# Performance work log

Measured on AMD Instinct MI355X. Metric: run time of the kernel, lower is better.

The kernel has to match this reference:

```python
import jax, jax.numpy as jnp
import numpy as np

N = 1024      # hidden_nodes (number of columns)
W = 128       # column_width
D = 1024      # input_dimension
F = W * N + N # per-column i-layer input size
SPARSITY = W / (W * (N - 1) + N) * 1.0  # modified_sparsity with total_neigbours=1


def setup_inputs() -> dict:
    key = jax.random.key(0)
    ks = jax.random.split(key, 10)
    s = lambda fan_in: 1.0 / np.sqrt(fan_in)
    x = jax.random.normal(ks[0], (D,), jnp.float32)
    hidden_state = jax.random.normal(ks[1], (N,), jnp.float32)
    W1 = jax.random.uniform(ks[2], (N, W, D), jnp.float32, -s(D), s(D))
    b1 = jax.random.uniform(ks[3], (N, W), jnp.float32, -s(D), s(D))
    W2 = jax.random.uniform(ks[4], (N, W, W), jnp.float32, -s(W), s(W))
    b2 = jax.random.uniform(ks[5], (N, W), jnp.float32, -s(W), s(W))
    Wi = jax.random.uniform(ks[6], (N, F), jnp.float32, -s(F), s(F))
    bi = jax.random.uniform(ks[7], (N,), jnp.float32, -s(F), s(F))
    # bernoulli mask, then force each column's own width-block to 1
    mask = (jax.random.uniform(ks[8], (N, F), jnp.float32) < SPARSITY).astype(jnp.float32)
    cols = jnp.arange(F)
    owner = jnp.where(cols < N * W, cols // W, -1)          # which column owns each feature slot
    block = (owner[None, :] == jnp.arange(N)[:, None]).astype(jnp.float32)
    mask = jnp.maximum(mask, block)
    pred = 0.1 * jax.random.normal(ks[9], (N,), jnp.float32)  # prediction_parameters ~ N(0, 0.1)
    return {"x": x, "hidden_state": hidden_state, "W1": W1, "b1": b1,
            "W2": W2, "b2": b2, "Wi": Wi, "bi": bi, "mask": mask, "pred": pred}


def reference(x, hidden_state, W1, b1, W2, b2, Wi, bi, mask, pred):
    # phase 1: per-column feature extractor (fc1 -> relu -> fc2 -> relu), batched over columns
    f1 = jax.nn.relu(jnp.einsum('nwd,d->nw', W1, x) + b1)        # [N, W]
    f2 = jax.nn.relu(jnp.einsum('nvw,nw->nv', W2, f1) + b2)      # [N, W]
    # phase 2: every column sees concat(all features, all hidden states)
    feat = jnp.concatenate([f2.reshape(-1), hidden_state])       # [F] = [N*W + N]
    i = jnp.tanh(jnp.einsum('nf,f->n', Wi * mask, feat) + bi)    # [N]
    h = hidden_state + i                                         # [N]
    y = jnp.sum(pred * h)                                        # scalar prediction
    return y, h
```

## Files before the change

kernel.cpp:

```cpp
#include <hip/hip_runtime.h>
#include <math.h>

#define NN 1024
#define WW 128
#define DD 1024
#define FF (NN * WW + NN)
#define NCHUNK 516
#define NWORD (NCHUNK * 4)

#define WS_BM_OFF  528384
#define WS_NEEDED  (WS_BM_OFF + (size_t)NN * NWORD * 8)

typedef float f32x4 __attribute__((ext_vector_type(4)));
typedef float f32x2 __attribute__((ext_vector_type(2)));

__device__ __forceinline__ f32x4 nt4(const float* p) {
    return __builtin_nontemporal_load(reinterpret_cast<const f32x4*>(p));
}
__device__ __forceinline__ f32x2 nt2(const float* p) {
    return __builtin_nontemporal_load(reinterpret_cast<const f32x2*>(p));
}
__device__ __forceinline__ float wred(float s) {
    #pragma unroll
    for (int m = 32; m > 0; m >>= 1) s += __shfl_xor(s, m, 64);
    return s;
}

__global__ __launch_bounds__(256) void colmlp(
    const float* __restrict__ x, const float* __restrict__ hidden,
    const float* __restrict__ W1, const float* __restrict__ b1,
    const float* __restrict__ W2, const float* __restrict__ b2,
    float* __restrict__ feat)
{
    __shared__ float f1_s[WW];
    const int n = blockIdx.x, tid = threadIdx.x, lane = tid & 63, w = tid >> 6;

    f32x4 xv0 = *reinterpret_cast<const f32x4*>(x +   0 + lane * 4);
    f32x4 xv1 = *reinterpret_cast<const f32x4*>(x + 256 + lane * 4);
    f32x4 xv2 = *reinterpret_cast<const f32x4*>(x + 512 + lane * 4);
    f32x4 xv3 = *reinterpret_cast<const f32x4*>(x + 768 + lane * 4);

    const float* W1n = W1 + (size_t)n * WW * DD;
    for (int g = 0; g < 4; ++g) {
        const float* rp = W1n + (size_t)(w * 32 + g * 8) * DD + lane * 4;
        float p[8];
        #pragma unroll
        for (int i = 0; i < 8; ++i) {
            const float* r = rp + (size_t)i * DD;
            f32x4 a = nt4(r) * xv0;
            a += nt4(r + 256) * xv1;
            a += nt4(r + 512) * xv2;
            a += nt4(r + 768) * xv3;
            p[i] = (a[0] + a[1]) + (a[2] + a[3]);
        }
        #pragma unroll
        for (int i = 0; i < 8; ++i) {
            const float s = wred(p[i]);
            if (lane == 0) {
                const int rr = w * 32 + g * 8 + i;
                const float v = s + b1[n * WW + rr];
                f1_s[rr] = v > 0.f ? v : 0.f;
            }
        }
    }
    __syncthreads();

    const float* W2n = W2 + (size_t)n * WW * WW;
    const f32x2 f1v = *reinterpret_cast<const f32x2*>(&f1_s[lane * 2]);
    for (int g = 0; g < 4; ++g) {
        float p[8];
        #pragma unroll
        for (int i = 0; i < 8; ++i) {
            const int rr = w * 32 + g * 8 + i;
            const f32x2 a = nt2(W2n + (size_t)rr * WW + lane * 2);
            p[i] = a[0] * f1v[0] + a[1] * f1v[1];
        }
        #pragma unroll
        for (int i = 0; i < 8; ++i) {
            const float s = wred(p[i]);
            if (lane == 0) {
                const int rr = w * 32 + g * 8 + i;
                const float v = s + b2[n * WW + rr];
                feat[n * WW + rr] = v > 0.f ? v : 0.f;
            }
        }
    }
    if (tid == 0) feat[NN * WW + n] = hidden[n];
}

__global__ __launch_bounds__(256) void maskscan(
    const float* __restrict__ mask, unsigned long long* __restrict__ bm)
{
    const int tid = threadIdx.x, lane = tid & 63, w = tid >> 6;
    const int wave_id = blockIdx.x * 4 + w;
    const int nwaves  = gridDim.x * 4;
    const int total   = NN * NCHUNK;
    #pragma unroll 2
    for (int c = wave_id; c < total; c += nwaves) {
        const f32x4 m = nt4(mask + (size_t)c * 256 + lane * 4);
        const unsigned long long b0 = __ballot(m[0] != 0.f);
        const unsigned long long b1 = __ballot(m[1] != 0.f);
        const unsigned long long b2 = __ballot(m[2] != 0.f);
        const unsigned long long b3 = __ballot(m[3] != 0.f);
        if (lane < 4) {
            const unsigned long long v = lane == 0 ? b0 : lane == 1 ? b1 : lane == 2 ? b2 : b3;
            bm[(size_t)c * 4 + lane] = v;
        }
    }
}

__global__ __launch_bounds__(256) void dotk(
    const unsigned long long* __restrict__ bm, const float* __restrict__ Wi,
    const float* __restrict__ feat, const float* __restrict__ bi,
    const float* __restrict__ hidden, float* __restrict__ out)
{
    const int n = blockIdx.x, tid = threadIdx.x;
    const unsigned long long* brow = bm + (size_t)n * NWORD;
    const float* wrow = Wi + (size_t)n * FF;
    float acc = 0.f;
    for (int wd = tid; wd < NWORD; wd += 256) {
        unsigned long long b = brow[wd];
        const int basef = (wd >> 2) * 256 + (wd & 3);
        while (b) {
            const int l = __builtin_ctzll(b);
            const int f = basef + l * 4;
            acc += wrow[f] * feat[f];
            b &= b - 1;
        }
    }
    acc = wred(acc);
    __shared__ float partial[4];
    if ((tid & 63) == 0) partial[tid >> 6] = acc;
    __syncthreads();
    if (tid == 0) {
        const float s = (partial[0] + partial[1]) + (partial[2] + partial[3]);
        out[1 + n] = hidden[n] + tanhf(s + bi[n]);
    }
}

__global__ __launch_bounds__(256) void predk(
    const float* __restrict__ pred, const float* __restrict__ h,
    float* __restrict__ out)
{
    const int tid = threadIdx.x;
    float acc = 0.f;
    for (int i = tid; i < NN; i += 256) acc += pred[i] * h[i];
    acc = wred(acc);
    __shared__ float partial[4];
    if ((tid & 63) == 0) partial[tid >> 6] = acc;
    __syncthreads();
    if (tid == 0) out[0] = (partial[0] + partial[1]) + (partial[2] + partial[3]);
}

__global__ __launch_bounds__(256) void feat_kernel(
    const float* __restrict__ x, const float* __restrict__ hidden,
    const float* __restrict__ W1, const float* __restrict__ b1,
    const float* __restrict__ W2, const float* __restrict__ b2,
    float* __restrict__ feat)
{
    const int n = blockIdx.x, tid = threadIdx.x, lane = tid & 63, wave = tid >> 6;
    __shared__ float x_s[DD];
    __shared__ float f1_s[WW];
    *reinterpret_cast<float4*>(x_s + tid * 4) = *reinterpret_cast<const float4*>(x + tid * 4);
    if (tid == 0) feat[NN * WW + n] = hidden[n];
    __syncthreads();
    const float* W1n = W1 + (size_t)n * WW * DD;
    for (int r = wave * 32; r < wave * 32 + 32; ++r) {
        const float* row = W1n + (size_t)r * DD;
        float4 acc = {0.f, 0.f, 0.f, 0.f};
        #pragma unroll
        for (int it = 0; it < 4; ++it) {
            const float4 a  = *reinterpret_cast<const float4*>(row + it * 256 + lane * 4);
            const float4 xv = *reinterpret_cast<const float4*>(x_s + it * 256 + lane * 4);
            acc.x += a.x * xv.x; acc.y += a.y * xv.y;
            acc.z += a.z * xv.z; acc.w += a.w * xv.w;
        }
        float s = wred((acc.x + acc.y) + (acc.z + acc.w));
        if (lane == 0) {
            float v = s + b1[n * WW + r];
            f1_s[r] = v > 0.f ? v : 0.f;
        }
    }
    __syncthreads();
    const float* W2n = W2 + (size_t)n * WW * WW;
    for (int r = wave * 32; r < wave * 32 + 32; ++r) {
        const float2 a = *reinterpret_cast<const float2*>(W2n + (size_t)r * WW + lane * 2);
        const float2 f = *reinterpret_cast<const float2*>(f1_s + lane * 2);
        float s = wred(a.x * f.x + a.y * f.y);
        if (lane == 0) {
            float v = s + b2[n * WW + r];
            feat[n * WW + r] = v > 0.f ? v : 0.f;
        }
    }
}

__global__ __launch_bounds__(256) void sparse_kernel(
    const float* __restrict__ Wi, const float* __restrict__ mask,
    const float* __restrict__ bi, const float* __restrict__ hidden,
    const float* __restrict__ feat, float* __restrict__ out)
{
    const int n = blockIdx.x, tid = threadIdx.x;
    const float* mrow = mask + (size_t)n * FF;
    const float* wrow = Wi   + (size_t)n * FF;
    float acc = 0.f;
    for (int it = 0; it < FF / 1024; ++it) {
        const int f = it * 1024 + tid * 4;
        const float4 m = *reinterpret_cast<const float4*>(mrow + f);
        if (m.x != 0.f) acc += wrow[f + 0] * m.x * feat[f + 0];
        if (m.y != 0.f) acc += wrow[f + 1] * m.y * feat[f + 1];
        if (m.z != 0.f) acc += wrow[f + 2] * m.z * feat[f + 2];
        if (m.w != 0.f) acc += wrow[f + 3] * m.w * feat[f + 3];
    }
    acc = wred(acc);
    __shared__ float partial[4];
    if ((tid & 63) == 0) partial[tid >> 6] = acc;
    __syncthreads();
    if (tid == 0) {
        const float s = (partial[0] + partial[1]) + (partial[2] + partial[3]);
        out[1 + n] = hidden[n] + tanhf(s + bi[n]);
    }
}

extern "C" void kernel_launch(void* const* d_in, const int* in_sizes, int n_in,
                              void* d_out, int out_size, void* d_ws, size_t ws_size,
                              hipStream_t stream) {
    const float* x      = (const float*)d_in[0];
    const float* hidden = (const float*)d_in[1];
    const float* W1     = (const float*)d_in[2];
    const float* b1     = (const float*)d_in[3];
    const float* W2     = (const float*)d_in[4];
    const float* b2     = (const float*)d_in[5];
    const float* Wi     = (const float*)d_in[6];
    const float* bi     = (const float*)d_in[7];
    const float* mask   = (const float*)d_in[8];
    const float* pred   = (const float*)d_in[9];

    float* out  = (float*)d_out;
    float* feat = (float*)d_ws;
    unsigned long long* bm = (unsigned long long*)((char*)d_ws + WS_BM_OFF);

    if (ws_size >= WS_NEEDED) {
        colmlp<<<NN, 256, 0, stream>>>(x, hidden, W1, b1, W2, b2, feat);
        maskscan<<<2048, 256, 0, stream>>>(mask, bm);
        dotk<<<NN, 256, 0, stream>>>(bm, Wi, feat, bi, hidden, out);
    } else {
        feat_kernel<<<NN, 256, 0, stream>>>(x, hidden, W1, b1, W2, b2, feat);
        sparse_kernel<<<NN, 256, 0, stream>>>(Wi, mask, bi, hidden, feat, out);
    }
    predk<<<1, 256, 0, stream>>>(pred, out + 1, out);
}
```

Before: 238.6 us.

## Fuse column MLP and mask bitmap scan into one interleaved launch

Merges the column-MLP kernel and the mask-to-bitmap scan kernel into a single 3072-block launch. Every third block computes one column's features, and the other two blocks per group each scan a contiguous range of mask chunks. The intent is to remove one kernel launch and its boundary and to let the compute-heavy W1 streaming overlap with the bandwidth-heavy mask scan. In exchange, each scanning wave now walks a fixed contiguous range with no loop unrolling, which replaces the earlier grid-stride pattern.

```diff
diff --git a/kernel.cpp b/kernel.cpp
--- a/kernel.cpp
+++ b/kernel.cpp
@@ -6,7 +6,9 @@
 #define DD 1024
 #define FF (NN * WW + NN)
 #define NCHUNK 516
+#define TOTCHUNK (NN * NCHUNK)
 #define NWORD (NCHUNK * 4)
+#define SCANWAVES 8192
 
 #define WS_BM_OFF  528384
 #define WS_NEEDED  (WS_BM_OFF + (size_t)NN * NWORD * 8)
@@ -26,14 +28,36 @@
     return s;
 }
 
-__global__ __launch_bounds__(256) void colmlp(
+__global__ __launch_bounds__(256) void fusedK(
     const float* __restrict__ x, const float* __restrict__ hidden,
     const float* __restrict__ W1, const float* __restrict__ b1,
     const float* __restrict__ W2, const float* __restrict__ b2,
-    float* __restrict__ feat)
-{
+    const float* __restrict__ mask,
+    float* __restrict__ feat, unsigned long long* __restrict__ bm)
+{
+    const int b = blockIdx.x, tid = threadIdx.x, lane = tid & 63, w = tid >> 6;
+
+    if (b % 3 != 0) {
+        const int sb = (b / 3) * 2 + (b % 3) - 1;
+        const int gw = sb * 4 + w;
+        const int cnt   = (gw < 4096) ? 65 : 64;
+        const int start = (gw < 4096) ? gw * 65 : 4096 * 65 + (gw - 4096) * 64;
+        for (int c = start; c < start + cnt; ++c) {
+            const f32x4 m = nt4(mask + (size_t)c * 256 + lane * 4);
+            const unsigned long long q0 = __ballot(m[0] != 0.f);
+            const unsigned long long q1 = __ballot(m[1] != 0.f);
+            const unsigned long long q2 = __ballot(m[2] != 0.f);
+            const unsigned long long q3 = __ballot(m[3] != 0.f);
+            if (lane < 4) {
+                const unsigned long long v = lane == 0 ? q0 : lane == 1 ? q1 : lane == 2 ? q2 : q3;
+                bm[(size_t)c * 4 + lane] = v;
+            }
+        }
+        return;
+    }
+
+    const int n = b / 3;
     __shared__ float f1_s[WW];
-    const int n = blockIdx.x, tid = threadIdx.x, lane = tid & 63, w = tid >> 6;
 
     f32x4 xv0 = *reinterpret_cast<const f32x4*>(x +   0 + lane * 4);
     f32x4 xv1 = *reinterpret_cast<const f32x4*>(x + 256 + lane * 4);
@@ -88,27 +112,6 @@
     if (tid == 0) feat[NN * WW + n] = hidden[n];
 }
 
-__global__ __launch_bounds__(256) void maskscan(
-    const float* __restrict__ mask, unsigned long long* __restrict__ bm)
-{
-    const int tid = threadIdx.x, lane = tid & 63, w = tid >> 6;
-    const int wave_id = blockIdx.x * 4 + w;
-    const int nwaves  = gridDim.x * 4;
-    const int total   = NN * NCHUNK;
-    #pragma unroll 2
-    for (int c = wave_id; c < total; c += nwaves) {
-        const f32x4 m = nt4(mask + (size_t)c * 256 + lane * 4);
-        const unsigned long long b0 = __ballot(m[0] != 0.f);
-        const unsigned long long b1 = __ballot(m[1] != 0.f);
-        const unsigned long long b2 = __ballot(m[2] != 0.f);
-        const unsigned long long b3 = __ballot(m[3] != 0.f);
-        if (lane < 4) {
-            const unsigned long long v = lane == 0 ? b0 : lane == 1 ? b1 : lane == 2 ? b2 : b3;
-            bm[(size_t)c * 4 + lane] = v;
-        }
-    }
-}
-
 __global__ __launch_bounds__(256) void dotk(
     const unsigned long long* __restrict__ bm, const float* __restrict__ Wi,
     const float* __restrict__ feat, const float* __restrict__ bi,
@@ -119,13 +122,13 @@
     const float* wrow = Wi + (size_t)n * FF;
     float acc = 0.f;
     for (int wd = tid; wd < NWORD; wd += 256) {
-        unsigned long long b = brow[wd];
+        unsigned long long q = brow[wd];
         const int basef = (wd >> 2) * 256 + (wd & 3);
-        while (b) {
-            const int l = __builtin_ctzll(b);
+        while (q) {
+            const int l = __builtin_ctzll(q);
             const int f = basef + l * 4;
             acc += wrow[f] * feat[f];
-            b &= b - 1;
+            q &= q - 1;
         }
     }
     acc = wred(acc);
@@ -240,8 +243,7 @@
     unsigned long long* bm = (unsigned long long*)((char*)d_ws + WS_BM_OFF);
 
     if (ws_size >= WS_NEEDED) {
-        colmlp<<<NN, 256, 0, stream>>>(x, hidden, W1, b1, W2, b2, feat);
-        maskscan<<<2048, 256, 0, stream>>>(mask, bm);
+        fusedK<<<3072, 256, 0, stream>>>(x, hidden, W1, b1, W2, b2, mask, feat, bm);
         dotk<<<NN, 256, 0, stream>>>(bm, Wi, feat, bi, hidden, out);
     } else {
         feat_kernel<<<NN, 256, 0, stream>>>(x, hidden, W1, b1, W2, b2, feat);
```

Measured after the change: 275.9 us. 15.6% more time.

## Split column MLP into flat-parallel W1 and W2 row-dot kernels

Applied to the files above, without the earlier changes.

Replaces the per-column colmlp kernel, which ran one block per column, with two grid-wide kernels. w1dot spreads W1 rows across 8192 waves, each handling pairs of rows with interleaved loads, and writes f1 to workspace. w2dot computes W2 rows with half-wave reductions that read f1 from global memory. The aim is better load balance and more memory-level parallelism on the W1 stream. In exchange it adds an extra launch, an f1 round trip through global memory and a larger workspace requirement.

```diff
diff --git a/kernel.cpp b/kernel.cpp
--- a/kernel.cpp
+++ b/kernel.cpp
@@ -5,11 +5,14 @@
 #define WW 128
 #define DD 1024
 #define FF (NN * WW + NN)
+#define NROW (NN * WW)
 #define NCHUNK 516
 #define NWORD (NCHUNK * 4)
+#define GWAVES 8192
 
 #define WS_BM_OFF  528384
-#define WS_NEEDED  (WS_BM_OFF + (size_t)NN * NWORD * 8)
+#define WS_F1_OFF  (WS_BM_OFF + (size_t)NN * NWORD * 8)
+#define WS_NEEDED  (WS_F1_OFF + (size_t)NROW * 4)
 
 typedef float f32x4 __attribute__((ext_vector_type(4)));
 typedef float f32x2 __attribute__((ext_vector_type(2)));
@@ -17,75 +20,79 @@
 __device__ __forceinline__ f32x4 nt4(const float* p) {
     return __builtin_nontemporal_load(reinterpret_cast<const f32x4*>(p));
 }
-__device__ __forceinline__ f32x2 nt2(const float* p) {
-    return __builtin_nontemporal_load(reinterpret_cast<const f32x2*>(p));
-}
 __device__ __forceinline__ float wred(float s) {
     #pragma unroll
     for (int m = 32; m > 0; m >>= 1) s += __shfl_xor(s, m, 64);
     return s;
 }
-
-__global__ __launch_bounds__(256) void colmlp(
-    const float* __restrict__ x, const float* __restrict__ hidden,
-    const float* __restrict__ W1, const float* __restrict__ b1,
+__device__ __forceinline__ float hred(float s) {
+    #pragma unroll
+    for (int m = 16; m > 0; m >>= 1) s += __shfl_xor(s, m, 64);
+    return s;
+}
+
+__global__ __launch_bounds__(256) void w1dot(
+    const float* __restrict__ x, const float* __restrict__ W1,
+    const float* __restrict__ b1, float* __restrict__ f1)
+{
+    const int tid = threadIdx.x, lane = tid & 63;
+    const int gw = blockIdx.x * 4 + (tid >> 6);
+
+    const f32x4 xv0 = *reinterpret_cast<const f32x4*>(x +   0 + lane * 4);
+    const f32x4 xv1 = *reinterpret_cast<const f32x4*>(x + 256 + lane * 4);
+    const f32x4 xv2 = *reinterpret_cast<const f32x4*>(x + 512 + lane * 4);
+    const f32x4 xv3 = *reinterpret_cast<const f32x4*>(x + 768 + lane * 4);
+
+    #pragma unroll
+    for (int i = 0; i < 8; ++i) {
+        const int r = (i * GWAVES + gw) * 2;
+        const float* rp = W1 + (size_t)r * DD + lane * 4;
+        f32x4 a0 = nt4(rp) * xv0;
+        f32x4 a1 = nt4(rp + DD) * xv0;
+        a0 += nt4(rp + 256) * xv1;
+        a1 += nt4(rp + DD + 256) * xv1;
+        a0 += nt4(rp + 512) * xv2;
+        a1 += nt4(rp + DD + 512) * xv2;
+        a0 += nt4(rp + 768) * xv3;
+        a1 += nt4(rp + DD + 768) * xv3;
+        float s0 = wred((a0[0] + a0[1]) + (a0[2] + a0[3]));
+        float s1 = wred((a1[0] + a1[1]) + (a1[2] + a1[3]));
+        if (lane == 0) {
+            const float v0 = s0 + b1[r];
+            const float v1 = s1 + b1[r + 1];
+            f1[r]     = v0 > 0.f ? v0 : 0.f;
+            f1[r + 1] = v1 > 0.f ? v1 : 0.f;
+        }
+    }
+}
+
+__global__ __launch_bounds__(256) void w2dot(
     const float* __restrict__ W2, const float* __restrict__ b2,
+    const float* __restrict__ f1, const float* __restrict__ hidden,
     float* __restrict__ feat)
 {
-    __shared__ float f1_s[WW];
-    const int n = blockIdx.x, tid = threadIdx.x, lane = tid & 63, w = tid >> 6;
-
-    f32x4 xv0 = *reinterpret_cast<const f32x4*>(x +   0 + lane * 4);
-    f32x4 xv1 = *reinterpret_cast<const f32x4*>(x + 256 + lane * 4);
-    f32x4 xv2 = *reinterpret_cast<const f32x4*>(x + 512 + lane * 4);
-    f32x4 xv3 = *reinterpret_cast<const f32x4*>(x + 768 + lane * 4);
-
-    const float* W1n = W1 + (size_t)n * WW * DD;
-    for (int g = 0; g < 4; ++g) {
-        const float* rp = W1n + (size_t)(w * 32 + g * 8) * DD + lane * 4;
-        float p[8];
-        #pragma unroll
-        for (int i = 0; i < 8; ++i) {
-            const float* r = rp + (size_t)i * DD;
-            f32x4 a = nt4(r) * xv0;
-            a += nt4(r + 256) * xv1;
-            a += nt4(r + 512) * xv2;
-            a += nt4(r + 768) * xv3;
-            p[i] = (a[0] + a[1]) + (a[2] + a[3]);
-        }
-        #pragma unroll
-        for (int i = 0; i < 8; ++i) {
-            const float s = wred(p[i]);
-            if (lane == 0) {
-                const int rr = w * 32 + g * 8 + i;
-                const float v = s + b1[n * WW + rr];
-                f1_s[rr] = v > 0.f ? v : 0.f;
-            }
-        }
-    }
-    __syncthreads();
-
-    const float* W2n = W2 + (size_t)n * WW * WW;
-    const f32x2 f1v = *reinterpret_cast<const f32x2*>(&f1_s[lane * 2]);
-    for (int g = 0; g < 4; ++g) {
-        float p[8];
-        #pragma unroll
-        for (int i = 0; i < 8; ++i) {
-            const int rr = w * 32 + g * 8 + i;
-            const f32x2 a = nt2(W2n + (size_t)rr * WW + lane * 2);
-            p[i] = a[0] * f1v[0] + a[1] * f1v[1];
-        }
-        #pragma unroll
-        for (int i = 0; i < 8; ++i) {
-            const float s = wred(p[i]);
-            if (lane == 0) {
-                const int rr = w * 32 + g * 8 + i;
-                const float v = s + b2[n * WW + rr];
-                feat[n * WW + rr] = v > 0.f ? v : 0.f;
-            }
-        }
-    }
-    if (tid == 0) feat[NN * WW + n] = hidden[n];
+    const int tid = threadIdx.x, lane = tid & 63;
+    const int gw = blockIdx.x * 4 + (tid >> 6);
+    const int gtid = blockIdx.x * 256 + tid;
+    if (gtid < NN) feat[NROW + gtid] = hidden[gtid];
+
+    #pragma unroll
+    for (int i = 0; i < 8; ++i) {
+        const int p  = i * GWAVES + gw;
+        const int rr = p * 2;
+        const int n  = p >> 6;
+        const f32x4 wv = nt4(W2 + (size_t)p * 256 + lane * 4);
+        const f32x4 fv = *reinterpret_cast<const f32x4*>(f1 + (n << 7) + ((lane & 31) << 2));
+        const f32x4 m = wv * fv;
+        const float s = hred((m[0] + m[1]) + (m[2] + m[3]));
+        if (lane == 0) {
+            const float v = s + b2[rr];
+            feat[rr] = v > 0.f ? v : 0.f;
+        } else if (lane == 32) {
+            const float v = s + b2[rr + 1];
+            feat[rr + 1] = v > 0.f ? v : 0.f;
+        }
+    }
 }
 
 __global__ __launch_bounds__(256) void maskscan(
@@ -98,12 +105,12 @@
     #pragma unroll 2
     for (int c = wave_id; c < total; c += nwaves) {
         const f32x4 m = nt4(mask + (size_t)c * 256 + lane * 4);
-        const unsigned long long b0 = __ballot(m[0] != 0.f);
-        const unsigned long long b1 = __ballot(m[1] != 0.f);
-        const unsigned long long b2 = __ballot(m[2] != 0.f);
-        const unsigned long long b3 = __ballot(m[3] != 0.f);
+        const unsigned long long q0 = __ballot(m[0] != 0.f);
+        const unsigned long long q1 = __ballot(m[1] != 0.f);
+        const unsigned long long q2 = __ballot(m[2] != 0.f);
+        const unsigned long long q3 = __ballot(m[3] != 0.f);
         if (lane < 4) {
-            const unsigned long long v = lane == 0 ? b0 : lane == 1 ? b1 : lane == 2 ? b2 : b3;
+            const unsigned long long v = lane == 0 ? q0 : lane == 1 ? q1 : lane == 2 ? q2 : q3;
             bm[(size_t)c * 4 + lane] = v;
         }
     }
@@ -119,13 +126,13 @@
     const float* wrow = Wi + (size_t)n * FF;
     float acc = 0.f;
     for (int wd = tid; wd < NWORD; wd += 256) {
-        unsigned long long b = brow[wd];
+        unsigned long long q = brow[wd];
         const int basef = (wd >> 2) * 256 + (wd & 3);
-        while (b) {
-            const int l = __builtin_ctzll(b);
+        while (q) {
+            const int l = __builtin_ctzll(q);
             const int f = basef + l * 4;
             acc += wrow[f] * feat[f];
-            b &= b - 1;
+            q &= q - 1;
         }
     }
     acc = wred(acc);
@@ -162,7 +169,7 @@
     __shared__ float x_s[DD];
     __shared__ float f1_s[WW];
     *reinterpret_cast<float4*>(x_s + tid * 4) = *reinterpret_cast<const float4*>(x + tid * 4);
-    if (tid == 0) feat[NN * WW + n] = hidden[n];
+    if (tid == 0) feat[NROW + n] = hidden[n];
     __syncthreads();
     const float* W1n = W1 + (size_t)n * WW * DD;
     for (int r = wave * 32; r < wave * 32 + 32; ++r) {
@@ -238,9 +245,11 @@
     float* out  = (float*)d_out;
     float* feat = (float*)d_ws;
     unsigned long long* bm = (unsigned long long*)((char*)d_ws + WS_BM_OFF);
+    float* f1 = (float*)((char*)d_ws + WS_F1_OFF);
 
     if (ws_size >= WS_NEEDED) {
-        colmlp<<<NN, 256, 0, stream>>>(x, hidden, W1, b1, W2, b2, feat);
+        w1dot<<<2048, 256, 0, stream>>>(x, W1, b1, f1);
+        w2dot<<<2048, 256, 0, stream>>>(W2, b2, f1, hidden, feat);
         maskscan<<<2048, 256, 0, stream>>>(mask, bm);
         dotk<<<NN, 256, 0, stream>>>(bm, Wi, feat, bi, hidden, out);
     } else {
```

Result: faster. 211.7 us (-11.3%).
